# Performance work log

Hardware: AMD Instinct MI355X
Metric: run time of the kernel (lower is better)

## Reference

```python
import jax, jax.numpy as jnp
import numpy as np

N_NODES = 100000
N_EDGES = 1600000
IN_CH, HID_CH, OUT_CH = 256, 128, 64


def setup_inputs() -> dict:
    key = jax.random.key(0)
    k_x, k_e, k1, k2, kb1, kb2 = jax.random.split(key, 6)
    x = jax.random.normal(k_x, (N_NODES, IN_CH), dtype=jnp.float32)
    edge_index = jax.random.randint(k_e, (2, N_EDGES), 0, N_NODES, dtype=jnp.int64)
    # Glorot-style init for GCN linear weights
    W1 = jax.random.normal(k1, (IN_CH, HID_CH), dtype=jnp.float32) * (1.0 / np.sqrt(IN_CH))
    b1 = jnp.zeros((HID_CH,), dtype=jnp.float32)
    W2 = jax.random.normal(k2, (HID_CH, OUT_CH), dtype=jnp.float32) * (1.0 / np.sqrt(HID_CH))
    b2 = jnp.zeros((OUT_CH,), dtype=jnp.float32)
    return {"x": x, "edge_index": edge_index, "W1": W1, "b1": b1, "W2": W2, "b2": b2}


def _gcn_norm(edge_index, n_nodes):
    # add self loops, compute D^{-1/2} (A+I) D^{-1/2} edge weights (PyG gcn_norm)
    loop = jnp.arange(n_nodes, dtype=edge_index.dtype)
    src = jnp.concatenate([edge_index[0], loop])
    dst = jnp.concatenate([edge_index[1], loop])
    deg = jax.ops.segment_sum(jnp.ones_like(src, dtype=jnp.float32), dst, num_segments=n_nodes)
    dinv = jnp.where(deg > 0, jax.lax.rsqrt(jnp.maximum(deg, 1.0)), 0.0)
    norm = dinv[src] * dinv[dst]  # [E + N]
    return src, dst, norm


def _gcn_conv(x, W, b, src, dst, norm, n_nodes):
    h = x @ W                         # linear first (PyG GCNConv)
    msg = norm[:, None] * h[src]      # gather + normalize  [E+N, out]
    agg = jax.ops.segment_sum(msg, dst, num_segments=n_nodes)
    return agg + b


def reference(x, edge_index, W1, b1, W2, b2):
    n = x.shape[0]
    src, dst, norm = _gcn_norm(edge_index, n)
    h = jax.nn.relu(_gcn_conv(x, W1, b1, src, dst, norm, n))
    # dropout is identity in eval mode
    z = _gcn_conv(h, W2, b2, src, dst, norm, n)
    # inner-product decoder on the provided edges, with sigmoid
    e_src, e_dst = edge_index[0], edge_index[1]
    logits = jnp.sum(z[e_src] * z[e_dst], axis=-1)
    return jax.nn.sigmoid(logits)
```

## Files before the change

### kernel.cpp

```cpp
#include <hip/hip_runtime.h>
#include <math.h>

#define N_NODES 100000
#define N_EDGES 1600000
#define IN_CH 256
#define HID_CH 128
#define OUT_CH 64
#define NB 1024
#define NPART 256
#define EPB (N_EDGES / NPART)
#define NB_USED ((N_NODES + 127) / 128)

typedef short s16x8 __attribute__((ext_vector_type(8)));
typedef unsigned short u16x8 __attribute__((ext_vector_type(8)));
typedef float f32x4 __attribute__((ext_vector_type(4)));

__device__ __forceinline__ float bf2f(unsigned short u) {
    union { unsigned int i; float f; } v;
    v.i = ((unsigned int)u) << 16;
    return v.f;
}
__device__ __forceinline__ unsigned short f2bf(float f) {
    union { float f; unsigned int i; } v;
    v.f = f;
    unsigned int u = v.i;
    return (unsigned short)((u + 0x7FFFu + ((u >> 16) & 1u)) >> 16);
}


__global__ __launch_bounds__(256) void k_hist(const int* __restrict__ dst,
                                              int* __restrict__ ghist) {
    __shared__ int h[NB];
    int b = blockIdx.x, t = threadIdx.x;
    for (int k = t; k < NB; k += 256) h[k] = 0;
    __syncthreads();
    int e0 = b * EPB;
    for (int e = e0 + t; e < e0 + EPB; e += 256)
        atomicAdd(&h[dst[e] >> 7], 1);
    __syncthreads();
    for (int k = t; k < NB; k += 256) ghist[k * NPART + b] = h[k];
}

__global__ __launch_bounds__(256) void k_scan_cols(const int* __restrict__ ghist,
                                                   int* __restrict__ goff,
                                                   int* __restrict__ btot) {
    __shared__ int tmp[NPART];
    int k = blockIdx.x, t = threadIdx.x;
    int v = ghist[k * NPART + t];
    tmp[t] = v;
    __syncthreads();
    for (int off = 1; off < NPART; off <<= 1) {
        int u = (t >= off) ? tmp[t - off] : 0;
        __syncthreads();
        tmp[t] += u;
        __syncthreads();
    }
    goff[k * NPART + t] = tmp[t] - v;
    if (t == NPART - 1) btot[k] = tmp[t];
}

__global__ __launch_bounds__(1024) void k_scan_base(const int* __restrict__ btot,
                                                    int* __restrict__ bbase) {
    __shared__ int tmp[NB];
    int t = threadIdx.x;
    int v = btot[t];
    tmp[t] = v;
    __syncthreads();
    for (int off = 1; off < NB; off <<= 1) {
        int u = (t >= off) ? tmp[t - off] : 0;
        __syncthreads();
        tmp[t] += u;
        __syncthreads();
    }
    bbase[t] = tmp[t] - v;
    if (t == NB - 1) bbase[NB] = tmp[t];
}

__global__ __launch_bounds__(256) void k_partition(const int* __restrict__ src,
                                                   const int* __restrict__ dst,
                                                   const int* __restrict__ goff,
                                                   const int* __restrict__ bbase,
                                                   int2* __restrict__ bsorted) {
    __shared__ int cur[NB];
    int b = blockIdx.x, t = threadIdx.x;
    for (int k = t; k < NB; k += 256) cur[k] = bbase[k] + goff[k * NPART + b];
    __syncthreads();
    int e0 = b * EPB;
    for (int e = e0 + t; e < e0 + EPB; e += 256) {
        int s = src[e], d = dst[e];
        int pos = atomicAdd(&cur[d >> 7], 1);
        bsorted[pos] = make_int2(s, d);
    }
}

__global__ __launch_bounds__(256) void k_bucket_csr(const int2* __restrict__ bsorted,
                                                    const int* __restrict__ bbase,
                                                    int* __restrict__ rowoff,
                                                    float* __restrict__ dinv,
                                                    int* __restrict__ csr_src) {
    __shared__ int cnt[128];
    __shared__ int tmp[256];
    __shared__ int cur[128];
    int b = blockIdx.x, t = threadIdx.x;
    int ebeg = bbase[b], eend = bbase[b + 1];
    if (t < 128) cnt[t] = 0;
    __syncthreads();
    for (int e = ebeg + t; e < eend; e += 256)
        atomicAdd(&cnt[bsorted[e].y & 127], 1);
    __syncthreads();
    int v = (t < 128) ? cnt[t] : 0;
    tmp[t] = v;
    __syncthreads();
    for (int off = 1; off < 256; off <<= 1) {
        int u = (t >= off) ? tmp[t - off] : 0;
        __syncthreads();
        tmp[t] += u;
        __syncthreads();
    }
    if (t < 128) {
        int base = ebeg + tmp[t] - v;
        cur[t] = base;
        int node = b * 128 + t;
        if (node < N_NODES) {
            rowoff[node] = base;
            dinv[node] = rsqrtf((float)v + 1.0f);
        }
    }
    __syncthreads();
    for (int e = ebeg + t; e < eend; e += 256) {
        int2 ed = bsorted[e];
        int pos = atomicAdd(&cur[ed.y & 127], 1);
        csr_src[pos] = ed.x;
    }
}


template <int K, int N>
__global__ void k_wt(const float* __restrict__ W, unsigned short* __restrict__ WT) {
    int t = blockIdx.x * blockDim.x + threadIdx.x;
    if (t >= K * N) return;
    int n = t / K;
    int k = t % K;
    WT[t] = f2bf(W[(size_t)k * N + n]);
}

__global__ __launch_bounds__(256, 2) void k_gemm1(const float* __restrict__ x,
                                                  const unsigned short* __restrict__ W1T,
                                                  const float* __restrict__ dinv,
                                                  unsigned short* __restrict__ hs1) {
    int tid = threadIdx.x;
    int w = tid >> 6;
    int lane = tid & 63;
    int l15 = lane & 15;
    int lhi = lane >> 4;
    int m0 = blockIdx.x * 64 + w * 16;

    int arow = m0 + l15;
    int arowc = (arow < N_NODES) ? arow : (N_NODES - 1);
    const float4* ap = reinterpret_cast<const float4*>(x + (size_t)arowc * IN_CH) + lhi * 2;

    float4 a[16];
    #pragma unroll
    for (int kk = 0; kk < 8; ++kk) {
        a[2 * kk]     = ap[kk * 8];
        a[2 * kk + 1] = ap[kk * 8 + 1];
    }
    __builtin_amdgcn_sched_barrier(0);

    s16x8 af[8];
    #pragma unroll
    for (int kk = 0; kk < 8; ++kk) {
        float4 a0 = a[2 * kk], a1 = a[2 * kk + 1];
        af[kk][0] = (short)f2bf(a0.x); af[kk][1] = (short)f2bf(a0.y);
        af[kk][2] = (short)f2bf(a0.z); af[kk][3] = (short)f2bf(a0.w);
        af[kk][4] = (short)f2bf(a1.x); af[kk][5] = (short)f2bf(a1.y);
        af[kk][6] = (short)f2bf(a1.z); af[kk][7] = (short)f2bf(a1.w);
    }

    f32x4 acc[8] = {};
    #pragma unroll
    for (int kk = 0; kk < 8; ++kk) {
        #pragma unroll
        for (int nt = 0; nt < 8; ++nt) {
            s16x8 bf = *reinterpret_cast<const s16x8*>(
                W1T + (size_t)(nt * 16 + l15) * IN_CH + kk * 32 + lhi * 8);
            acc[nt] = __builtin_amdgcn_mfma_f32_16x16x32_bf16(af[kk], bf, acc[nt], 0, 0, 0);
        }
    }

    float dv[4];
    int rb = m0 + lhi * 4;
    #pragma unroll
    for (int r = 0; r < 4; ++r) dv[r] = (rb + r < N_NODES) ? dinv[rb + r] : 0.0f;
    #pragma unroll
    for (int nt = 0; nt < 8; ++nt) {
        #pragma unroll
        for (int r = 0; r < 4; ++r) {
            int row = rb + r;
            if (row < N_NODES)
                hs1[(size_t)row * HID_CH + nt * 16 + l15] = f2bf(dv[r] * acc[nt][r]);
        }
    }
}

__global__ __launch_bounds__(256) void k_gemm2(const unsigned short* __restrict__ h1r,
                                               const unsigned short* __restrict__ W2T,
                                               const float* __restrict__ dinv,
                                               unsigned short* __restrict__ hs2) {
    int tid = threadIdx.x;
    int w = tid >> 6;
    int lane = tid & 63;
    int l15 = lane & 15;
    int lhi = lane >> 4;
    int m0 = blockIdx.x * 64 + w * 16;

    int arow = m0 + l15;
    int arowc = (arow < N_NODES) ? arow : (N_NODES - 1);
    const s16x8* ap = reinterpret_cast<const s16x8*>(h1r + (size_t)arowc * HID_CH) + lhi;

    s16x8 af[4];
    #pragma unroll
    for (int kk = 0; kk < 4; ++kk) af[kk] = ap[kk * 4];
    __builtin_amdgcn_sched_barrier(0);

    f32x4 acc[4] = {};
    #pragma unroll
    for (int kk = 0; kk < 4; ++kk) {
        #pragma unroll
        for (int nt = 0; nt < 4; ++nt) {
            s16x8 bf = *reinterpret_cast<const s16x8*>(
                W2T + (size_t)(nt * 16 + l15) * HID_CH + kk * 32 + lhi * 8);
            acc[nt] = __builtin_amdgcn_mfma_f32_16x16x32_bf16(af[kk], bf, acc[nt], 0, 0, 0);
        }
    }

    float dv[4];
    int rb = m0 + lhi * 4;
    #pragma unroll
    for (int r = 0; r < 4; ++r) dv[r] = (rb + r < N_NODES) ? dinv[rb + r] : 0.0f;
    #pragma unroll
    for (int nt = 0; nt < 4; ++nt) {
        #pragma unroll
        for (int r = 0; r < 4; ++r) {
            int row = rb + r;
            if (row < N_NODES)
                hs2[(size_t)row * OUT_CH + nt * 16 + l15] = f2bf(dv[r] * acc[nt][r]);
        }
    }
}

template <int C, bool RELU>
__global__ __launch_bounds__(256) void k_gather_agg(const int* __restrict__ rowoff,
                                                    const int* __restrict__ csr_src,
                                                    const unsigned short* __restrict__ hs,
                                                    const float* __restrict__ dinv,
                                                    const float* __restrict__ b,
                                                    unsigned short* __restrict__ outp) {
    constexpr int TPN = C / 8;
    constexpr int NPB = 256 / TPN;
    int t = threadIdx.x;
    int node = blockIdx.x * NPB + t / TPN;
    int q = t % TPN;
    if (node >= N_NODES) return;

    int beg = rowoff[node];
    int end = (node + 1 < N_NODES) ? rowoff[node + 1] : N_EDGES;

    float acc[8];
    {
        u16x8 sv = *reinterpret_cast<const u16x8*>(&hs[(size_t)node * C + q * 8]);
        #pragma unroll
        for (int j = 0; j < 8; ++j) acc[j] = bf2f(sv[j]);
    }

    int i = beg;
    for (; i + 1 < end; i += 2) {
        int s0 = csr_src[i];
        int s1 = csr_src[i + 1];
        u16x8 v0 = *reinterpret_cast<const u16x8*>(&hs[(size_t)s0 * C + q * 8]);
        u16x8 v1 = *reinterpret_cast<const u16x8*>(&hs[(size_t)s1 * C + q * 8]);
        #pragma unroll
        for (int j = 0; j < 8; ++j) acc[j] += bf2f(v0[j]) + bf2f(v1[j]);
    }
    if (i < end) {
        int s0 = csr_src[i];
        u16x8 v0 = *reinterpret_cast<const u16x8*>(&hs[(size_t)s0 * C + q * 8]);
        #pragma unroll
        for (int j = 0; j < 8; ++j) acc[j] += bf2f(v0[j]);
    }

    float w = dinv[node];
    float4 b0 = reinterpret_cast<const float4*>(b)[q * 2];
    float4 b1 = reinterpret_cast<const float4*>(b)[q * 2 + 1];
    float bb[8] = {b0.x, b0.y, b0.z, b0.w, b1.x, b1.y, b1.z, b1.w};
    u16x8 o;
    #pragma unroll
    for (int j = 0; j < 8; ++j) {
        float v = w * acc[j] + bb[j];
        if (RELU) v = fmaxf(v, 0.0f);
        o[j] = f2bf(v);
    }
    *reinterpret_cast<u16x8*>(&outp[(size_t)node * C + q * 8]) = o;
}


__global__ __launch_bounds__(256) void k_decode(const int* __restrict__ esrc,
                                                const int* __restrict__ edst,
                                                const unsigned short* __restrict__ z,
                                                float* __restrict__ out) {
    int tid = threadIdx.x;
    int e = blockIdx.x * 32 + tid / 8;
    int q = tid % 8;
    if (e >= N_EDGES) return;
    int s = esrc[e], d = edst[e];
    u16x8 a = *reinterpret_cast<const u16x8*>(&z[(size_t)s * OUT_CH + q * 8]);
    u16x8 b = *reinterpret_cast<const u16x8*>(&z[(size_t)d * OUT_CH + q * 8]);
    float dot = 0.0f;
    #pragma unroll
    for (int j = 0; j < 8; ++j) dot += bf2f(a[j]) * bf2f(b[j]);
    dot += __shfl_xor(dot, 1);
    dot += __shfl_xor(dot, 2);
    dot += __shfl_xor(dot, 4);
    if (q == 0) out[e] = 1.0f / (1.0f + expf(-dot));
}


extern "C" void kernel_launch(void* const* d_in, const int* in_sizes, int n_in,
                              void* d_out, int out_size, void* d_ws, size_t ws_size,
                              hipStream_t stream) {
    const float* x  = (const float*)d_in[0];
    const int*   ei = (const int*)d_in[1];
    const float* W1 = (const float*)d_in[2];
    const float* b1 = (const float*)d_in[3];
    const float* W2 = (const float*)d_in[4];
    const float* b2 = (const float*)d_in[5];
    float* out = (float*)d_out;

    const int* src = ei;
    const int* dst = ei + N_EDGES;

    char* ws = (char*)d_ws;
    int*   ghist   = (int*)(ws + 0x000000);
    int*   goff    = (int*)(ws + 0x100000);
    int*   btot    = (int*)(ws + 0x200000);
    int*   bbase   = (int*)(ws + 0x202000);
    int*   rowoff  = (int*)(ws + 0x210000);
    float* dinv    = (float*)(ws + 0x290000);
    unsigned short* W1T = (unsigned short*)(ws + 0x310000);
    unsigned short* W2T = (unsigned short*)(ws + 0x320000);
    int*   csr_src = (int*)(ws + 0x400000);
    int2*  bsorted = (int2*)(ws + 0xC00000);
    unsigned short* hs1 = (unsigned short*)(ws + 0x1900000);
    unsigned short* h1r = (unsigned short*)(ws + 0x3200000);
    unsigned short* hs2 = (unsigned short*)(ws + 0x4B00000);
    unsigned short* z   = (unsigned short*)(ws + 0x5800000);

    k_hist<<<NPART, 256, 0, stream>>>(dst, ghist);
    k_scan_cols<<<NB, 256, 0, stream>>>(ghist, goff, btot);
    k_scan_base<<<1, NB, 0, stream>>>(btot, bbase);
    k_partition<<<NPART, 256, 0, stream>>>(src, dst, goff, bbase, bsorted);
    k_bucket_csr<<<NB_USED, 256, 0, stream>>>(bsorted, bbase, rowoff, dinv, csr_src);

    k_wt<IN_CH, HID_CH><<<(IN_CH * HID_CH + 255) / 256, 256, 0, stream>>>(W1, W1T);
    k_wt<HID_CH, OUT_CH><<<(HID_CH * OUT_CH + 255) / 256, 256, 0, stream>>>(W2, W2T);

    k_gemm1<<<(N_NODES + 63) / 64, 256, 0, stream>>>(x, W1T, dinv, hs1);
    k_gather_agg<HID_CH, true><<<(N_NODES * 16 + 255) / 256, 256, 0, stream>>>(
        rowoff, csr_src, hs1, dinv, b1, h1r);

    k_gemm2<<<(N_NODES + 63) / 64, 256, 0, stream>>>(h1r, W2T, dinv, hs2);
    k_gather_agg<OUT_CH, false><<<(N_NODES * 8 + 255) / 256, 256, 0, stream>>>(
        rowoff, csr_src, hs2, dinv, b2, z);

    k_decode<<<N_EDGES / 32, 256, 0, stream>>>(src, dst, z, out);
}
```

Baseline: 295.3 us.

## Stage MFMA-fragment-ordered weights in LDS and use persistent grid-stride GEMM blocks

```diff
diff --git a/kernel.cpp b/kernel.cpp
--- a/kernel.cpp
+++ b/kernel.cpp
@@ -6,6 +6,7 @@
 #define IN_CH 256
 #define HID_CH 128
 #define OUT_CH 64
+#define NTILES ((N_NODES + 63) / 64)
 #define NB 1024
 #define NPART 256
 #define EPB (N_EDGES / NPART)
@@ -134,117 +135,156 @@
     }
 }
 
-
-template <int K, int N>
-__global__ void k_wt(const float* __restrict__ W, unsigned short* __restrict__ WT) {
-    int t = blockIdx.x * blockDim.x + threadIdx.x;
-    if (t >= K * N) return;
-    int n = t / K;
-    int k = t % K;
-    WT[t] = f2bf(W[(size_t)k * N + n]);
+__global__ void k_wt1(const float* __restrict__ W1, unsigned short* __restrict__ Wf1) {
+    int u = blockIdx.x * 256 + threadIdx.x;
+    int f = u >> 6, lane = u & 63;
+    int kk = f >> 3, nt = f & 7;
+    int l15 = lane & 15, lhi = lane >> 4;
+    int n = nt * 16 + l15;
+    int kbase = kk * 32 + lhi * 8;
+    #pragma unroll
+    for (int j = 0; j < 8; ++j)
+        Wf1[(size_t)u * 8 + j] = f2bf(W1[(size_t)(kbase + j) * HID_CH + n]);
+}
+
+__global__ void k_wt2(const float* __restrict__ W2, unsigned short* __restrict__ Wf2) {
+    int u = blockIdx.x * 256 + threadIdx.x;
+    int f = u >> 6, lane = u & 63;
+    int kk = f >> 2, nt = f & 3;
+    int l15 = lane & 15, lhi = lane >> 4;
+    int n = nt * 16 + l15;
+    int kbase = kk * 32 + lhi * 8;
+    #pragma unroll
+    for (int j = 0; j < 8; ++j)
+        Wf2[(size_t)u * 8 + j] = f2bf(W2[(size_t)(kbase + j) * OUT_CH + n]);
 }
 
 __global__ __launch_bounds__(256, 2) void k_gemm1(const float* __restrict__ x,
-                                                  const unsigned short* __restrict__ W1T,
+                                                  const unsigned short* __restrict__ Wf1,
                                                   const float* __restrict__ dinv,
                                                   unsigned short* __restrict__ hs1) {
+    __shared__ unsigned short Wlds[32768];
     int tid = threadIdx.x;
     int w = tid >> 6;
     int lane = tid & 63;
     int l15 = lane & 15;
     int lhi = lane >> 4;
-    int m0 = blockIdx.x * 64 + w * 16;
-
-    int arow = m0 + l15;
-    int arowc = (arow < N_NODES) ? arow : (N_NODES - 1);
-    const float4* ap = reinterpret_cast<const float4*>(x + (size_t)arowc * IN_CH) + lhi * 2;
-
-    float4 a[16];
-    #pragma unroll
-    for (int kk = 0; kk < 8; ++kk) {
-        a[2 * kk]     = ap[kk * 8];
-        a[2 * kk + 1] = ap[kk * 8 + 1];
-    }
-    __builtin_amdgcn_sched_barrier(0);
-
-    s16x8 af[8];
-    #pragma unroll
-    for (int kk = 0; kk < 8; ++kk) {
-        float4 a0 = a[2 * kk], a1 = a[2 * kk + 1];
-        af[kk][0] = (short)f2bf(a0.x); af[kk][1] = (short)f2bf(a0.y);
-        af[kk][2] = (short)f2bf(a0.z); af[kk][3] = (short)f2bf(a0.w);
-        af[kk][4] = (short)f2bf(a1.x); af[kk][5] = (short)f2bf(a1.y);
-        af[kk][6] = (short)f2bf(a1.z); af[kk][7] = (short)f2bf(a1.w);
-    }
-
-    f32x4 acc[8] = {};
-    #pragma unroll
-    for (int kk = 0; kk < 8; ++kk) {
+
+    #pragma unroll
+    for (int i = 0; i < 16; ++i) {
+        const unsigned short* gp = Wf1 + (size_t)(i * 256 + tid) * 8;
+        unsigned short* lp = Wlds + i * 2048 + w * 512;
+        __builtin_amdgcn_global_load_lds(
+            (const __attribute__((address_space(1))) void*)gp,
+            (__attribute__((address_space(3))) void*)lp, 16, 0, 0);
+    }
+    asm volatile("s_waitcnt vmcnt(0)");
+    __syncthreads();
+
+    for (int mt = blockIdx.x; mt < NTILES; mt += gridDim.x) {
+        int m0 = mt * 64;
+        int arow = m0 + w * 16 + l15;
+        int arowc = (arow < N_NODES) ? arow : (N_NODES - 1);
+        const float4* ap = reinterpret_cast<const float4*>(x + (size_t)arowc * IN_CH) + lhi * 2;
+
+        float4 a[16];
+        #pragma unroll
+        for (int kk = 0; kk < 8; ++kk) {
+            a[2 * kk]     = ap[kk * 8];
+            a[2 * kk + 1] = ap[kk * 8 + 1];
+        }
+        s16x8 af[8];
+        #pragma unroll
+        for (int kk = 0; kk < 8; ++kk) {
+            float4 a0 = a[2 * kk], a1 = a[2 * kk + 1];
+            af[kk][0] = (short)f2bf(a0.x); af[kk][1] = (short)f2bf(a0.y);
+            af[kk][2] = (short)f2bf(a0.z); af[kk][3] = (short)f2bf(a0.w);
+            af[kk][4] = (short)f2bf(a1.x); af[kk][5] = (short)f2bf(a1.y);
+            af[kk][6] = (short)f2bf(a1.z); af[kk][7] = (short)f2bf(a1.w);
+        }
+
+        f32x4 acc[8] = {};
+        #pragma unroll
+        for (int kk = 0; kk < 8; ++kk) {
+            #pragma unroll
+            for (int nt = 0; nt < 8; ++nt) {
+                s16x8 bf = *reinterpret_cast<const s16x8*>(
+                    &Wlds[(kk * 8 + nt) * 512 + lane * 8]);
+                acc[nt] = __builtin_amdgcn_mfma_f32_16x16x32_bf16(af[kk], bf, acc[nt], 0, 0, 0);
+            }
+        }
+
+        float dv[4];
+        int rb = m0 + w * 16 + lhi * 4;
+        #pragma unroll
+        for (int r = 0; r < 4; ++r) dv[r] = (rb + r < N_NODES) ? dinv[rb + r] : 0.0f;
         #pragma unroll
         for (int nt = 0; nt < 8; ++nt) {
-            s16x8 bf = *reinterpret_cast<const s16x8*>(
-                W1T + (size_t)(nt * 16 + l15) * IN_CH + kk * 32 + lhi * 8);
-            acc[nt] = __builtin_amdgcn_mfma_f32_16x16x32_bf16(af[kk], bf, acc[nt], 0, 0, 0);
-        }
-    }
-
-    float dv[4];
-    int rb = m0 + lhi * 4;
-    #pragma unroll
-    for (int r = 0; r < 4; ++r) dv[r] = (rb + r < N_NODES) ? dinv[rb + r] : 0.0f;
-    #pragma unroll
-    for (int nt = 0; nt < 8; ++nt) {
-        #pragma unroll
-        for (int r = 0; r < 4; ++r) {
-            int row = rb + r;
-            if (row < N_NODES)
-                hs1[(size_t)row * HID_CH + nt * 16 + l15] = f2bf(dv[r] * acc[nt][r]);
-        }
-    }
-}
-
-__global__ __launch_bounds__(256) void k_gemm2(const unsigned short* __restrict__ h1r,
-                                               const unsigned short* __restrict__ W2T,
-                                               const float* __restrict__ dinv,
-                                               unsigned short* __restrict__ hs2) {
+            #pragma unroll
+            for (int r = 0; r < 4; ++r) {
+                int row = rb + r;
+                if (row < N_NODES)
+                    hs1[(size_t)row * HID_CH + nt * 16 + l15] = f2bf(dv[r] * acc[nt][r]);
+            }
+        }
+    }
+}
+
+__global__ __launch_bounds__(256, 4) void k_gemm2(const unsigned short* __restrict__ h1r,
+                                                  const unsigned short* __restrict__ Wf2,
+                                                  const float* __restrict__ dinv,
+                                                  unsigned short* __restrict__ hs2) {
+    __shared__ unsigned short Wlds[8192];
     int tid = threadIdx.x;
     int w = tid >> 6;
     int lane = tid & 63;
     int l15 = lane & 15;
     int lhi = lane >> 4;
-    int m0 = blockIdx.x * 64 + w * 16;
-
-    int arow = m0 + l15;
-    int arowc = (arow < N_NODES) ? arow : (N_NODES - 1);
-    const s16x8* ap = reinterpret_cast<const s16x8*>(h1r + (size_t)arowc * HID_CH) + lhi;
-
-    s16x8 af[4];
-    #pragma unroll
-    for (int kk = 0; kk < 4; ++kk) af[kk] = ap[kk * 4];
-    __builtin_amdgcn_sched_barrier(0);
-
-    f32x4 acc[4] = {};
-    #pragma unroll
-    for (int kk = 0; kk < 4; ++kk) {
+
+    #pragma unroll
+    for (int i = 0; i < 4; ++i) {
+        const unsigned short* gp = Wf2 + (size_t)(i * 256 + tid) * 8;
+        unsigned short* lp = Wlds + i * 2048 + w * 512;
+        __builtin_amdgcn_global_load_lds(
+            (const __attribute__((address_space(1))) void*)gp,
+            (__attribute__((address_space(3))) void*)lp, 16, 0, 0);
+    }
+    asm volatile("s_waitcnt vmcnt(0)");
+    __syncthreads();
+
+    for (int mt = blockIdx.x; mt < NTILES; mt += gridDim.x) {
+        int m0 = mt * 64;
+        int arow = m0 + w * 16 + l15;
+        int arowc = (arow < N_NODES) ? arow : (N_NODES - 1);
+        const s16x8* ap = reinterpret_cast<const s16x8*>(h1r + (size_t)arowc * HID_CH) + lhi;
+
+        s16x8 af[4];
+        #pragma unroll
+        for (int kk = 0; kk < 4; ++kk) af[kk] = ap[kk * 4];
+
+        f32x4 acc[4] = {};
+        #pragma unroll
+        for (int kk = 0; kk < 4; ++kk) {
+            #pragma unroll
+            for (int nt = 0; nt < 4; ++nt) {
+                s16x8 bf = *reinterpret_cast<const s16x8*>(
+                    &Wlds[(kk * 4 + nt) * 512 + lane * 8]);
+                acc[nt] = __builtin_amdgcn_mfma_f32_16x16x32_bf16(af[kk], bf, acc[nt], 0, 0, 0);
+            }
+        }
+
+        float dv[4];
+        int rb = m0 + w * 16 + lhi * 4;
+        #pragma unroll
+        for (int r = 0; r < 4; ++r) dv[r] = (rb + r < N_NODES) ? dinv[rb + r] : 0.0f;
         #pragma unroll
         for (int nt = 0; nt < 4; ++nt) {
-            s16x8 bf = *reinterpret_cast<const s16x8*>(
-                W2T + (size_t)(nt * 16 + l15) * HID_CH + kk * 32 + lhi * 8);
-            acc[nt] = __builtin_amdgcn_mfma_f32_16x16x32_bf16(af[kk], bf, acc[nt], 0, 0, 0);
-        }
-    }
-
-    float dv[4];
-    int rb = m0 + lhi * 4;
-    #pragma unroll
-    for (int r = 0; r < 4; ++r) dv[r] = (rb + r < N_NODES) ? dinv[rb + r] : 0.0f;
-    #pragma unroll
-    for (int nt = 0; nt < 4; ++nt) {
-        #pragma unroll
-        for (int r = 0; r < 4; ++r) {
-            int row = rb + r;
-            if (row < N_NODES)
-                hs2[(size_t)row * OUT_CH + nt * 16 + l15] = f2bf(dv[r] * acc[nt][r]);
+            #pragma unroll
+            for (int r = 0; r < 4; ++r) {
+                int row = rb + r;
+                if (row < N_NODES)
+                    hs2[(size_t)row * OUT_CH + nt * 16 + l15] = f2bf(dv[r] * acc[nt][r]);
+            }
         }
     }
 }
@@ -346,8 +386,8 @@
     int*   bbase   = (int*)(ws + 0x202000);
     int*   rowoff  = (int*)(ws + 0x210000);
     float* dinv    = (float*)(ws + 0x290000);
-    unsigned short* W1T = (unsigned short*)(ws + 0x310000);
-    unsigned short* W2T = (unsigned short*)(ws + 0x320000);
+    unsigned short* Wf1 = (unsigned short*)(ws + 0x310000);
+    unsigned short* Wf2 = (unsigned short*)(ws + 0x320000);
     int*   csr_src = (int*)(ws + 0x400000);
     int2*  bsorted = (int2*)(ws + 0xC00000);
     unsigned short* hs1 = (unsigned short*)(ws + 0x1900000);
@@ -361,14 +401,14 @@
     k_partition<<<NPART, 256, 0, stream>>>(src, dst, goff, bbase, bsorted);
     k_bucket_csr<<<NB_USED, 256, 0, stream>>>(bsorted, bbase, rowoff, dinv, csr_src);
 
-    k_wt<IN_CH, HID_CH><<<(IN_CH * HID_CH + 255) / 256, 256, 0, stream>>>(W1, W1T);
-    k_wt<HID_CH, OUT_CH><<<(HID_CH * OUT_CH + 255) / 256, 256, 0, stream>>>(W2, W2T);
-
-    k_gemm1<<<(N_NODES + 63) / 64, 256, 0, stream>>>(x, W1T, dinv, hs1);
+    k_wt1<<<16, 256, 0, stream>>>(W1, Wf1);
+    k_wt2<<<4, 256, 0, stream>>>(W2, Wf2);
+
+    k_gemm1<<<512, 256, 0, stream>>>(x, Wf1, dinv, hs1);
     k_gather_agg<HID_CH, true><<<(N_NODES * 16 + 255) / 256, 256, 0, stream>>>(
         rowoff, csr_src, hs1, dinv, b1, h1r);
 
-    k_gemm2<<<(N_NODES + 63) / 64, 256, 0, stream>>>(h1r, W2T, dinv, hs2);
+    k_gemm2<<<1024, 256, 0, stream>>>(h1r, Wf2, dinv, hs2);
     k_gather_agg<OUT_CH, false><<<(N_NODES * 8 + 255) / 256, 256, 0, stream>>>(
         rowoff, csr_src, hs2, dinv, b2, z);
 
```

After: 276.0 us. 6.5% less time.
